# Performance work log

Measured on AMD Instinct MI355X. Metric: run time of the kernel, lower is better.

Reference implementation:

```python
import jax, jax.numpy as jnp
import numpy as np


def setup_inputs() -> dict:
    key = jax.random.key(0)
    k1, k2 = jax.random.split(key)
    B, C, T = 8, 256, 2048
    n_q, bins = 8, 1024
    x = jax.random.normal(k1, (B, C, T), dtype=jnp.float32)
    codebook = jax.random.normal(k2, (n_q, bins, C), dtype=jnp.float32)
    return {"x": x, "codebook": codebook, "sample_rate": 24000, "bandwidth": 6}


def reference(x, codebook, sample_rate, bandwidth):
    B, C, T = x.shape
    n_q, bins, _ = codebook.shape
    # flatten frames: (B, C, T) -> (B*T, C)
    x_flat = jnp.transpose(x, (0, 2, 1)).reshape(-1, C)
    # the expanded (N, n_q, bins, C) subtraction, without materializing it)
    x2 = jnp.sum(x_flat * x_flat, axis=-1)[:, None, None]          # (N, 1, 1)
    c2 = jnp.sum(codebook * codebook, axis=-1)[None]               # (1, n_q, bins)
    xc = jnp.einsum('nd,qbd->nqb', x_flat, codebook)               # (N, n_q, bins)
    distances = x2 + c2 - 2.0 * xc
    indices = jnp.argmin(distances, axis=-1)                       # (N, n_q)
    # gather one code per quantizer level and sum (matches the python loop)
    gathered = codebook[jnp.arange(n_q)[None, :], indices]         # (N, n_q, C)
    quant_flat = jnp.sum(gathered, axis=1)                         # (N, C)
    quantized = jnp.transpose(quant_flat.reshape(B, T, C), (0, 2, 1))
    commitment_loss = jnp.mean((jax.lax.stop_gradient(quantized) - x) ** 2)
    codebook_loss = jnp.mean((quantized - jax.lax.stop_gradient(x)) ** 2)
    loss = commitment_loss + codebook_loss
    q_ste = x + jax.lax.stop_gradient(quantized - x)               # straight-through
    return q_ste, indices, loss
```

## Files before the change

### kernel.cpp

```cpp
#include <hip/hip_runtime.h>

typedef unsigned long long u64;
typedef unsigned int u32;
typedef _Float16 f16;
typedef f16 f16x8 __attribute__((ext_vector_type(8)));
typedef float f32x4 __attribute__((ext_vector_type(4)));

#define B_   8
#define C_   256
#define T_   2048
#define NQ   8
#define BINS 1024
#define NROWS (B_ * T_)
#define KA   256
#define KB   256
#define NTILE 16

#define XS_OFF   ((size_t)0)
#define CS_OFF   ((size_t)8388608)
#define XT_OFF   ((size_t)12582912)
#define C2D_OFF  ((size_t)29360128)
#define C2K_OFF  ((size_t)29425664)
#define IDXI_OFF ((size_t)29458432)

static __device__ __forceinline__ void gll16(const void* g, void* l) {
    __builtin_amdgcn_global_load_lds(
        (const __attribute__((address_space(1))) u32*)g,
        (__attribute__((address_space(3))) u32*)l, 16, 0, 0);
}

__global__ __launch_bounds__(256)
void prep_x(const float* __restrict__ x, float* __restrict__ x_t,
            f16* __restrict__ xs) {
    __shared__ float tile[64][65];
    const int tid = threadIdx.x;
    const int bid = blockIdx.x;
    const int b  = bid >> 7;
    const int c0 = ((bid >> 5) & 3) * 64;
    const int t0 = (bid & 31) * 64;
    {
        const int j = tid & 63, cg = tid >> 6;
        #pragma unroll
        for (int ii = 0; ii < 16; ++ii) {
            const int cl = cg * 16 + ii;
            tile[cl][j] = x[((size_t)(b * C_ + c0 + cl) * T_) + t0 + j];
        }
    }
    __syncthreads();
    {
        const int cl = tid & 63, tg = tid >> 6;
        #pragma unroll
        for (int jj = 0; jj < 16; ++jj) {
            const int tl = tg * 16 + jj;
            const float v = tile[cl][tl];
            const size_t n = (size_t)b * T_ + t0 + tl;
            x_t[n * C_ + c0 + cl] = v;
            xs[n * KA + c0 + cl]  = (f16)v;
        }
    }
}

struct alignas(8) H4 { f16 v[4]; };
__global__ __launch_bounds__(256)
void prep_cb_c2(const float* __restrict__ cb, f16* __restrict__ cs,
                double* __restrict__ c2d, float* __restrict__ c2k) {
    const int w    = threadIdx.x >> 6;
    const int lane = threadIdx.x & 63;
    const int code = blockIdx.x * 4 + w;
    const float4 v = *(const float4*)(cb + (size_t)code * C_ + lane * 4);
    H4 h;
    h.v[0] = (f16)v.x; h.v[1] = (f16)v.y; h.v[2] = (f16)v.z; h.v[3] = (f16)v.w;
    *(H4*)(cs + (size_t)code * KB + lane * 4) = h;
    double s = (double)v.x * v.x + (double)v.y * v.y +
               (double)v.z * v.z + (double)v.w * v.w;
    #pragma unroll
    for (int off = 32; off; off >>= 1) s += __shfl_down(s, off, 64);
    if (lane == 0) {
        c2d[code] = s;
        c2k[code] = (float)s + 1000.0f;
    }
}

__global__ __launch_bounds__(1024)
void dist_kernel(const f16* __restrict__ xs, const f16* __restrict__ cs,
                 const float* __restrict__ c2k, const float* __restrict__ x_t,
                 const float* __restrict__ cb, const double* __restrict__ c2d,
                 float* __restrict__ idx_f, int* __restrict__ idx_i) {
    __shared__ f16 Bs[2][64][256];
    __shared__ u32 red[128][8];

    const int tid  = threadIdx.x;
    const int lane = tid & 63;
    const int w    = tid >> 6;
    const int wr   = w >> 2;
    const int wc   = w & 3;
    const int bid  = blockIdx.x;
    const int q    = bid & 7;
    const int rt   = bid >> 3;
    const int n0   = rt * 128;

    const int c = lane & 15;
    const int g = lane >> 4;

    f16x8 af[2][8];
    {
        const f16* pa = xs + (size_t)(n0 + wr * 32 + c) * KA + g * 8;
        #pragma unroll
        for (int m = 0; m < 2; ++m)
            #pragma unroll
            for (int kk = 0; kk < 8; ++kk)
                af[m][kk] = *(const f16x8*)(pa + m * 16 * KA + kk * 32);
    }

    const int crow  = tid >> 5;
    const int slotl = (tid & 31) ^ (crow & 7);
    const f16* pb = cs + (size_t)q * 1024 * KB;
    const int wbase = w * 512;

    #define STAGE(buf, t)                                                    \
        do {                                                                 \
            f16* b0 = &Bs[buf][0][0];                                        \
            const f16* s_ = pb + (size_t)((t) * 64 + crow) * KB + slotl * 8; \
            gll16(s_,            b0 + wbase);                                \
            gll16(s_ + 32 * KB,  b0 + 8192 + wbase);                         \
        } while (0)

    u32 k1[2][4], k2[2][4];
    #pragma unroll
    for (int m = 0; m < 2; ++m)
        #pragma unroll
        for (int r = 0; r < 4; ++r) { k1[m][r] = ~0u; k2[m][r] = ~0u; }

    const float* c2q = c2k + q * BINS;
    const int rowoff = (wc * 16 + c) * 256;
    const int sw = c & 7;

    STAGE(0, 0);
    __syncthreads();

    #pragma unroll 1
    for (int t = 0; t < NTILE; ++t) {
        const int buf = t & 1;
        if (t < NTILE - 1) STAGE(buf ^ 1, t + 1);

        f32x4 acc[2];
        #pragma unroll
        for (int m = 0; m < 2; ++m) {
            f32x4 z = {0.f, 0.f, 0.f, 0.f};
            acc[m] = z;
        }

        const f16* bb = &Bs[buf][0][0] + rowoff;
        #pragma unroll
        for (int half = 0; half < 2; ++half) {
            f16x8 bg[4];
            #pragma unroll
            for (int k4 = 0; k4 < 4; ++k4) {
                const int kk = half * 4 + k4;
                bg[k4] = *(const f16x8*)(bb + ((kk * 4 + g) ^ sw) * 8);
            }
            #pragma unroll
            for (int k4 = 0; k4 < 4; ++k4)
                #pragma unroll
                for (int m = 0; m < 2; ++m)
                    acc[m] = __builtin_amdgcn_mfma_f32_16x16x32_f16(
                        af[m][half * 4 + k4], bg[k4], acc[m], 0, 0, 0);
        }

        const int codeL = t * 64 + wc * 16 + c;
        const float cc = c2q[codeL];
        #pragma unroll
        for (int m = 0; m < 2; ++m)
            #pragma unroll
            for (int r = 0; r < 4; ++r) {
                const float sc = fmaf(-2.f, acc[m][r], cc);
                const u32 key = (__float_as_uint(sc) & 0xFFFFFC00u) | (u32)codeL;
                const u32 hi = k1[m][r] > key ? k1[m][r] : key;
                k1[m][r] = k1[m][r] < key ? k1[m][r] : key;
                k2[m][r] = k2[m][r] < hi ? k2[m][r] : hi;
            }

        __syncthreads();
    }
    #undef STAGE

    #pragma unroll
    for (int m = 0; m < 2; ++m)
        #pragma unroll
        for (int r = 0; r < 4; ++r) {
            u32 a1 = k1[m][r], a2 = k2[m][r];
            #pragma unroll
            for (int mask = 1; mask <= 8; mask <<= 1) {
                const u32 o1 = __shfl_xor(a1, mask, 64);
                const u32 o2 = __shfl_xor(a2, mask, 64);
                const u32 hi = a1 > o1 ? a1 : o1;
                a1 = a1 < o1 ? a1 : o1;
                const u32 lo2 = o2 < a2 ? o2 : a2;
                a2 = hi < lo2 ? hi : lo2;
            }
            if (c == 0) {
                const int rowl = wr * 32 + m * 16 + g * 4 + r;
                red[rowl][wc * 2]     = a1;
                red[rowl][wc * 2 + 1] = a2;
            }
        }
    __syncthreads();

    if (tid < 128) {
        u32 s0 = ~0u, s1 = ~0u, s2 = ~0u, s3 = ~0u;
        #pragma unroll
        for (int jj = 0; jj < 8; ++jj) {
            const u32 k = red[tid][jj];
            if (k < s0)      { s3 = s2; s2 = s1; s1 = s0; s0 = k; }
            else if (k < s1) { s3 = s2; s2 = s1; s1 = k; }
            else if (k < s2) { s3 = s2; s2 = k; }
            else if (k < s3) { s3 = k; }
        }
        red[tid][0] = s0 & 1023u;
        red[tid][1] = s1 & 1023u;
        red[tid][2] = s2 & 1023u;
        red[tid][3] = s3 & 1023u;
    }
    __syncthreads();

    {
        const int cand = lane >> 4;
        const int cg   = lane & 15;
        #pragma unroll 1
        for (int i = 0; i < 8; ++i) {
            const int rl = w * 8 + i;
            const int n  = n0 + rl;
            const int bin = (int)red[rl][cand];
            const float* xr = x_t + (size_t)n * C_ + cg * 16;
            const float* cr = cb + ((size_t)(q * BINS + bin)) * C_ + cg * 16;
            double d = 0.0;
            #pragma unroll
            for (int u = 0; u < 4; ++u) {
                const float4 xv = *(const float4*)(xr + u * 4);
                const float4 cv = *(const float4*)(cr + u * 4);
                d += (double)xv.x * cv.x + (double)xv.y * cv.y
                   + (double)xv.z * cv.z + (double)xv.w * cv.w;
            }
            #pragma unroll
            for (int off = 8; off; off >>= 1) d += __shfl_down(d, off, 16);
            const double dist = c2d[q * BINS + bin] - 2.0 * d;
            const double d0 = __shfl(dist,  0, 64);
            const double d1 = __shfl(dist, 16, 64);
            const double d2 = __shfl(dist, 32, 64);
            const double d3 = __shfl(dist, 48, 64);
            if (lane == 0) {
                const int b0 = (int)red[rl][0], b1 = (int)red[rl][1];
                const int b2 = (int)red[rl][2], b3 = (int)red[rl][3];
                double best = d0;
                int win = b0;
                if (d1 < best || (d1 == best && b1 < win)) { best = d1; win = b1; }
                if (d2 < best || (d2 == best && b2 < win)) { best = d2; win = b2; }
                if (d3 < best || (d3 == best && b3 < win)) { best = d3; win = b3; }
                idx_f[(size_t)n * NQ + q] = (float)win;
                idx_i[(size_t)n * NQ + q] = win;
            }
        }
    }
}

__global__ __launch_bounds__(256)
void gather_kernel(const float* __restrict__ x, const float* __restrict__ cb,
                   const int* __restrict__ idx_i, float* __restrict__ out,
                   float* __restrict__ loss) {
    __shared__ float ql[C_][17];
    const int blk = blockIdx.x;
    const int b   = blk >> 7;
    const int t0  = (blk & 127) << 4;
    const int tid = threadIdx.x;
    {
        const int c = tid;
        for (int nl = 0; nl < 16; ++nl) {
            const int n = b * T_ + t0 + nl;
            float acc = 0.f;
            #pragma unroll
            for (int qq = 0; qq < NQ; ++qq) {
                const int id = idx_i[(size_t)n * NQ + qq];
                acc += cb[((size_t)qq * BINS + id) * C_ + c];
            }
            ql[c][nl] = acc;
        }
    }
    __syncthreads();
    const int tx = tid & 15, ty = tid >> 4;
    float lsum = 0.f;
    for (int cg = 0; cg < 16; ++cg) {
        const int c = cg * 16 + ty;
        const size_t off = ((size_t)b * C_ + c) * T_ + t0 + tx;
        const float qv = ql[c][tx];
        const float xv = x[off];
        out[off] = qv;
        const float d = qv - xv;
        lsum += d * d;
    }
    #pragma unroll
    for (int off = 32; off; off >>= 1) lsum += __shfl_down(lsum, off, 64);
    if ((tid & 63) == 0)
        atomicAdd(loss, lsum * (2.0f / (float)(B_ * C_ * T_)));
}

extern "C" void kernel_launch(void* const* d_in, const int* in_sizes, int n_in,
                              void* d_out, int out_size, void* d_ws, size_t ws_size,
                              hipStream_t stream) {
    const float* x  = (const float*)d_in[0];
    const float* cb = (const float*)d_in[1];

    float* out   = (float*)d_out;
    float* idx_f = out + (size_t)B_ * C_ * T_;
    float* loss  = idx_f + (size_t)NROWS * NQ;

    char* ws = (char*)d_ws;
    f16*    xs    = (f16*)(ws + XS_OFF);
    f16*    cs    = (f16*)(ws + CS_OFF);
    float*  x_t   = (float*)(ws + XT_OFF);
    double* c2d   = (double*)(ws + C2D_OFF);
    float*  c2k   = (float*)(ws + C2K_OFF);
    int*    idx_i = (int*)(ws + IDXI_OFF);

    hipMemsetAsync(loss, 0, sizeof(float), stream);
    prep_x<<<1024, 256, 0, stream>>>(x, x_t, xs);
    prep_cb_c2<<<2048, 256, 0, stream>>>(cb, cs, c2d, c2k);
    dist_kernel<<<1024, 1024, 0, stream>>>(xs, cs, c2k, x_t, cb, c2d,
                                           idx_f, idx_i);
    gather_kernel<<<B_ * (T_ / 16), 256, 0, stream>>>(x, cb, idx_i, out, loss);
}
```

Before: 261.5 us.

## Widen per-wave row tiles and skip fp64 rescoring when top-2 gap is large

The distance kernel now runs 512 threads per block, with each wave computing four 16-row MFMA tiles instead of two. This reuses each staged codebook fragment across more rows, and the codebook tile is staged with four loads per thread. After the top-4 reduction, a flag records whether the fp16 top-2 score gap is within a fixed margin. When it is not, the exact fp64 rescoring of candidates is skipped and the best fp16 candidate is written directly. This trades a small risk of misranked indices when the fp16 error exceeds the margin for less rescoring work, along with lower wave count per block.

```diff
diff --git a/kernel.cpp b/kernel.cpp
--- a/kernel.cpp
+++ b/kernel.cpp
@@ -15,6 +15,7 @@
 #define KA   256
 #define KB   256
 #define NTILE 16
+#define MARGIN 3.0f
 
 #define XS_OFF   ((size_t)0)
 #define CS_OFF   ((size_t)8388608)
@@ -81,7 +82,7 @@
     }
 }
 
-__global__ __launch_bounds__(1024)
+__global__ __launch_bounds__(512)
 void dist_kernel(const f16* __restrict__ xs, const f16* __restrict__ cs,
                  const float* __restrict__ c2k, const float* __restrict__ x_t,
                  const float* __restrict__ cb, const double* __restrict__ c2d,
@@ -102,32 +103,35 @@
     const int c = lane & 15;
     const int g = lane >> 4;
 
-    f16x8 af[2][8];
-    {
-        const f16* pa = xs + (size_t)(n0 + wr * 32 + c) * KA + g * 8;
-        #pragma unroll
-        for (int m = 0; m < 2; ++m)
+    f16x8 af[4][8];
+    {
+        const f16* pa = xs + (size_t)(n0 + wr * 64 + c) * KA + g * 8;
+        #pragma unroll
+        for (int m = 0; m < 4; ++m)
             #pragma unroll
             for (int kk = 0; kk < 8; ++kk)
                 af[m][kk] = *(const f16x8*)(pa + m * 16 * KA + kk * 32);
     }
 
-    const int crow  = tid >> 5;
-    const int slotl = (tid & 31) ^ (crow & 7);
-    const f16* pb = cs + (size_t)q * 1024 * KB;
-    const int wbase = w * 512;
+    const int crow0 = tid >> 5;
+    const int slotl = (tid & 31) ^ (crow0 & 7);
+    const f16* srcb = cs + (size_t)q * 1024 * KB + (size_t)crow0 * KB
+                         + slotl * 8;
+    const int dstw = w * 512;
 
     #define STAGE(buf, t)                                                    \
         do {                                                                 \
-            f16* b0 = &Bs[buf][0][0];                                        \
-            const f16* s_ = pb + (size_t)((t) * 64 + crow) * KB + slotl * 8; \
-            gll16(s_,            b0 + wbase);                                \
-            gll16(s_ + 32 * KB,  b0 + 8192 + wbase);                         \
+            f16* b0 = &Bs[buf][0][0] + dstw;                                 \
+            const f16* s_ = srcb + (size_t)(t) * 64 * KB;                    \
+            gll16(s_,                 b0);                                   \
+            gll16(s_ + 16 * KB,       b0 + 4096);                            \
+            gll16(s_ + 32 * KB,       b0 + 8192);                            \
+            gll16(s_ + 48 * KB,       b0 + 12288);                           \
         } while (0)
 
-    u32 k1[2][4], k2[2][4];
+    u32 k1[4][4], k2[4][4];
     #pragma unroll
-    for (int m = 0; m < 2; ++m)
+    for (int m = 0; m < 4; ++m)
         #pragma unroll
         for (int r = 0; r < 4; ++r) { k1[m][r] = ~0u; k2[m][r] = ~0u; }
 
@@ -143,9 +147,9 @@
         const int buf = t & 1;
         if (t < NTILE - 1) STAGE(buf ^ 1, t + 1);
 
-        f32x4 acc[2];
-        #pragma unroll
-        for (int m = 0; m < 2; ++m) {
+        f32x4 acc[4];
+        #pragma unroll
+        for (int m = 0; m < 4; ++m) {
             f32x4 z = {0.f, 0.f, 0.f, 0.f};
             acc[m] = z;
         }
@@ -162,7 +166,7 @@
             #pragma unroll
             for (int k4 = 0; k4 < 4; ++k4)
                 #pragma unroll
-                for (int m = 0; m < 2; ++m)
+                for (int m = 0; m < 4; ++m)
                     acc[m] = __builtin_amdgcn_mfma_f32_16x16x32_f16(
                         af[m][half * 4 + k4], bg[k4], acc[m], 0, 0, 0);
         }
@@ -170,7 +174,7 @@
         const int codeL = t * 64 + wc * 16 + c;
         const float cc = c2q[codeL];
         #pragma unroll
-        for (int m = 0; m < 2; ++m)
+        for (int m = 0; m < 4; ++m)
             #pragma unroll
             for (int r = 0; r < 4; ++r) {
                 const float sc = fmaf(-2.f, acc[m][r], cc);
@@ -185,7 +189,7 @@
     #undef STAGE
 
     #pragma unroll
-    for (int m = 0; m < 2; ++m)
+    for (int m = 0; m < 4; ++m)
         #pragma unroll
         for (int r = 0; r < 4; ++r) {
             u32 a1 = k1[m][r], a2 = k2[m][r];
@@ -199,7 +203,7 @@
                 a2 = hi < lo2 ? hi : lo2;
             }
             if (c == 0) {
-                const int rowl = wr * 32 + m * 16 + g * 4 + r;
+                const int rowl = wr * 64 + m * 16 + g * 4 + r;
                 red[rowl][wc * 2]     = a1;
                 red[rowl][wc * 2 + 1] = a2;
             }
@@ -216,10 +220,13 @@
             else if (k < s2) { s3 = s2; s2 = k; }
             else if (k < s3) { s3 = k; }
         }
+        const float f0 = __uint_as_float(s0 & 0xFFFFFC00u);
+        const float f1 = __uint_as_float(s1 & 0xFFFFFC00u);
         red[tid][0] = s0 & 1023u;
         red[tid][1] = s1 & 1023u;
         red[tid][2] = s2 & 1023u;
         red[tid][3] = s3 & 1023u;
+        red[tid][4] = (f1 - f0 <= MARGIN) ? 1u : 0u;
     }
     __syncthreads();
 
@@ -227,9 +234,17 @@
         const int cand = lane >> 4;
         const int cg   = lane & 15;
         #pragma unroll 1
-        for (int i = 0; i < 8; ++i) {
-            const int rl = w * 8 + i;
+        for (int i = 0; i < 16; ++i) {
+            const int rl = w * 16 + i;
             const int n  = n0 + rl;
+            if (!red[rl][4]) {
+                if (lane == 0) {
+                    const int win = (int)red[rl][0];
+                    idx_f[(size_t)n * NQ + q] = (float)win;
+                    idx_i[(size_t)n * NQ + q] = win;
+                }
+                continue;
+            }
             const int bin = (int)red[rl][cand];
             const float* xr = x_t + (size_t)n * C_ + cg * 16;
             const float* cr = cb + ((size_t)(q * BINS + bin)) * C_ + cg * 16;
@@ -324,7 +339,7 @@
     hipMemsetAsync(loss, 0, sizeof(float), stream);
     prep_x<<<1024, 256, 0, stream>>>(x, x_t, xs);
     prep_cb_c2<<<2048, 256, 0, stream>>>(cb, cs, c2d, c2k);
-    dist_kernel<<<1024, 1024, 0, stream>>>(xs, cs, c2k, x_t, cb, c2d,
-                                           idx_f, idx_i);
+    dist_kernel<<<1024, 512, 0, stream>>>(xs, cs, c2k, x_t, cb, c2d,
+                                          idx_f, idx_i);
     gather_kernel<<<B_ * (T_ / 16), 256, 0, stream>>>(x, cb, idx_i, out, loss);
 }
```

Result: faster. 231.6 us (-11.4%).

## Skip exact fp64 rescoring when fp16 top-two gap exceeds margin; merge prep kernels

Applied to the files above, without the earlier changes.

After the fp16 MFMA distance pass, each row records whether the gap between the best and second-best approximate distance is within a fixed margin. Rows with a clear winner skip the fp64 recomputation over the four candidates and write the top index directly. The two preprocessing kernels are also merged into one launch to save a kernel launch. The fixed margin assumes the fp16 distance error stays below it, which depends on input scale and could pick the wrong index for other data.

```diff
diff --git a/kernel.cpp b/kernel.cpp
--- a/kernel.cpp
+++ b/kernel.cpp
@@ -15,6 +15,7 @@
 #define KA   256
 #define KB   256
 #define NTILE 16
+#define MARGIN 3.0f
 
 #define XS_OFF   ((size_t)0)
 #define CS_OFF   ((size_t)8388608)
@@ -29,55 +30,56 @@
         (__attribute__((address_space(3))) u32*)l, 16, 0, 0);
 }
 
+struct alignas(8) H4 { f16 v[4]; };
 __global__ __launch_bounds__(256)
-void prep_x(const float* __restrict__ x, float* __restrict__ x_t,
-            f16* __restrict__ xs) {
-    __shared__ float tile[64][65];
+void prep_all(const float* __restrict__ x, float* __restrict__ x_t,
+              f16* __restrict__ xs, const float* __restrict__ cb,
+              f16* __restrict__ cs, double* __restrict__ c2d,
+              float* __restrict__ c2k) {
     const int tid = threadIdx.x;
     const int bid = blockIdx.x;
-    const int b  = bid >> 7;
-    const int c0 = ((bid >> 5) & 3) * 64;
-    const int t0 = (bid & 31) * 64;
-    {
-        const int j = tid & 63, cg = tid >> 6;
-        #pragma unroll
-        for (int ii = 0; ii < 16; ++ii) {
-            const int cl = cg * 16 + ii;
-            tile[cl][j] = x[((size_t)(b * C_ + c0 + cl) * T_) + t0 + j];
-        }
-    }
-    __syncthreads();
-    {
-        const int cl = tid & 63, tg = tid >> 6;
-        #pragma unroll
-        for (int jj = 0; jj < 16; ++jj) {
-            const int tl = tg * 16 + jj;
-            const float v = tile[cl][tl];
-            const size_t n = (size_t)b * T_ + t0 + tl;
-            x_t[n * C_ + c0 + cl] = v;
-            xs[n * KA + c0 + cl]  = (f16)v;
-        }
-    }
-}
-
-struct alignas(8) H4 { f16 v[4]; };
-__global__ __launch_bounds__(256)
-void prep_cb_c2(const float* __restrict__ cb, f16* __restrict__ cs,
-                double* __restrict__ c2d, float* __restrict__ c2k) {
-    const int w    = threadIdx.x >> 6;
-    const int lane = threadIdx.x & 63;
-    const int code = blockIdx.x * 4 + w;
-    const float4 v = *(const float4*)(cb + (size_t)code * C_ + lane * 4);
-    H4 h;
-    h.v[0] = (f16)v.x; h.v[1] = (f16)v.y; h.v[2] = (f16)v.z; h.v[3] = (f16)v.w;
-    *(H4*)(cs + (size_t)code * KB + lane * 4) = h;
-    double s = (double)v.x * v.x + (double)v.y * v.y +
-               (double)v.z * v.z + (double)v.w * v.w;
-    #pragma unroll
-    for (int off = 32; off; off >>= 1) s += __shfl_down(s, off, 64);
-    if (lane == 0) {
-        c2d[code] = s;
-        c2k[code] = (float)s + 1000.0f;
+    if (bid < 1024) {
+        __shared__ float tile[64][65];
+        const int b  = bid >> 7;
+        const int c0 = ((bid >> 5) & 3) * 64;
+        const int t0 = (bid & 31) * 64;
+        {
+            const int j = tid & 63, cg = tid >> 6;
+            #pragma unroll
+            for (int ii = 0; ii < 16; ++ii) {
+                const int cl = cg * 16 + ii;
+                tile[cl][j] = x[((size_t)(b * C_ + c0 + cl) * T_) + t0 + j];
+            }
+        }
+        __syncthreads();
+        {
+            const int cl = tid & 63, tg = tid >> 6;
+            #pragma unroll
+            for (int jj = 0; jj < 16; ++jj) {
+                const int tl = tg * 16 + jj;
+                const float v = tile[cl][tl];
+                const size_t n = (size_t)b * T_ + t0 + tl;
+                x_t[n * C_ + c0 + cl] = v;
+                xs[n * KA + c0 + cl]  = (f16)v;
+            }
+        }
+    } else {
+        const int w    = tid >> 6;
+        const int lane = tid & 63;
+        const int code = (bid - 1024) * 4 + w;
+        const float4 v = *(const float4*)(cb + (size_t)code * C_ + lane * 4);
+        H4 h;
+        h.v[0] = (f16)v.x; h.v[1] = (f16)v.y;
+        h.v[2] = (f16)v.z; h.v[3] = (f16)v.w;
+        *(H4*)(cs + (size_t)code * KB + lane * 4) = h;
+        double s = (double)v.x * v.x + (double)v.y * v.y +
+                   (double)v.z * v.z + (double)v.w * v.w;
+        #pragma unroll
+        for (int off = 32; off; off >>= 1) s += __shfl_down(s, off, 64);
+        if (lane == 0) {
+            c2d[code] = s;
+            c2k[code] = (float)s + 1000.0f;
+        }
     }
 }
 
@@ -121,8 +123,8 @@
         do {                                                                 \
             f16* b0 = &Bs[buf][0][0];                                        \
             const f16* s_ = pb + (size_t)((t) * 64 + crow) * KB + slotl * 8; \
-            gll16(s_,            b0 + wbase);                                \
-            gll16(s_ + 32 * KB,  b0 + 8192 + wbase);                         \
+            gll16(s_,            b0 + wbase);                                 \
+            gll16(s_ + 32 * KB,  b0 + 8192 + wbase);                          \
         } while (0)
 
     u32 k1[2][4], k2[2][4];
@@ -216,10 +218,13 @@
             else if (k < s2) { s3 = s2; s2 = k; }
             else if (k < s3) { s3 = k; }
         }
+        const float f0 = __uint_as_float(s0 & 0xFFFFFC00u);
+        const float f1 = __uint_as_float(s1 & 0xFFFFFC00u);
         red[tid][0] = s0 & 1023u;
         red[tid][1] = s1 & 1023u;
         red[tid][2] = s2 & 1023u;
         red[tid][3] = s3 & 1023u;
+        red[tid][4] = (f1 - f0 <= MARGIN) ? 1u : 0u;
     }
     __syncthreads();
 
@@ -230,6 +235,14 @@
         for (int i = 0; i < 8; ++i) {
             const int rl = w * 8 + i;
             const int n  = n0 + rl;
+            if (!red[rl][4]) {
+                if (lane == 0) {
+                    const int win = (int)red[rl][0];
+                    idx_f[(size_t)n * NQ + q] = (float)win;
+                    idx_i[(size_t)n * NQ + q] = win;
+                }
+                continue;
+            }
             const int bin = (int)red[rl][cand];
             const float* xr = x_t + (size_t)n * C_ + cg * 16;
             const float* cr = cb + ((size_t)(q * BINS + bin)) * C_ + cg * 16;
@@ -322,8 +335,7 @@
     int*    idx_i = (int*)(ws + IDXI_OFF);
 
     hipMemsetAsync(loss, 0, sizeof(float), stream);
-    prep_x<<<1024, 256, 0, stream>>>(x, x_t, xs);
-    prep_cb_c2<<<2048, 256, 0, stream>>>(cb, cs, c2d, c2k);
+    prep_all<<<3072, 256, 0, stream>>>(x, x_t, xs, cb, cs, c2d, c2k);
     dist_kernel<<<1024, 1024, 0, stream>>>(xs, cs, c2k, x_t, cb, c2d,
                                            idx_f, idx_i);
     gather_kernel<<<B_ * (T_ / 16), 256, 0, stream>>>(x, cb, idx_i, out, loss);
```

Measured after the change: 215.2 us, median of 2. 17.7% less time.
